# Kernel tuning notes

Hardware: AMD Instinct MI355X
Metric: run time of the kernel (lower is better)

Reference implementation:

```python
import jax, jax.numpy as jnp
import numpy as np

B, L, C = 2, 2048, 1024
DK, H = 64, 16

def setup_inputs() -> dict:
    key = jax.random.key(0)
    ks = jax.random.split(key, 12)
    def lin(kw, kb, out_dim, in_dim):
        w = jax.random.normal(kw, (out_dim, in_dim), jnp.float32) * (1.0 / np.sqrt(in_dim))
        b = jnp.zeros((out_dim,), jnp.float32)
        return w, b
    WQ_w, WQ_b = lin(ks[0], ks[1], DK * H, C)
    WK_w, WK_b = lin(ks[2], ks[3], DK * H, C)
    WV_w, WV_b = lin(ks[4], ks[5], DK * H, C)
    WO_w, WO_b = lin(ks[6], ks[7], C, DK * H)
    qx = jax.random.normal(ks[8], (B, L, C), jnp.float32)
    kx = jax.random.normal(ks[9], (B, L, C), jnp.float32)
    vx = jax.random.normal(ks[10], (B, L, C), jnp.float32)
    maskPAD = jax.random.randint(ks[11], (B, L, L), 0, 2, jnp.int32)
    return {"qx": qx, "kx": kx, "vx": vx, "maskPAD": maskPAD,
            "WQ_w": WQ_w, "WQ_b": WQ_b, "WK_w": WK_w, "WK_b": WK_b,
            "WV_w": WV_w, "WV_b": WV_b, "WO_w": WO_w, "WO_b": WO_b}

def reference(qx, kx, vx, maskPAD, WQ_w, WQ_b, WK_w, WK_b, WV_w, WV_b, WO_w, WO_b):
    Bq, qL, _ = qx.shape
    kvL = kx.shape[1]
    # projections -> [B, H, L, DK]
    q = (qx @ WQ_w.T + WQ_b).reshape(Bq, qL, H, DK).transpose(0, 2, 1, 3)
    k = (kx @ WK_w.T + WK_b).reshape(Bq, kvL, H, DK).transpose(0, 2, 1, 3)
    v = (vx @ WV_w.T + WV_b).reshape(Bq, kvL, H, DK).transpose(0, 2, 1, 3)
    scores = jnp.einsum('bhqd,bhkd->bhqk', q, k) / np.sqrt(DK).astype(np.float32)
    scores = jnp.where((maskPAD == 0)[:, None, :, :], jnp.float32(-2**15 + 1), scores)
    alpha = jax.nn.softmax(scores, axis=3)  # dropout p=0 (eval)
    z = jnp.einsum('bhqk,bhkd->bhqd', alpha, v)
    z = z.transpose(0, 2, 1, 3).reshape(Bq, qL, H * DK)
    return z @ WO_w.T + WO_b
```

## Files before the change

### kernel.cpp

```cpp
#include <hip/hip_runtime.h>
#include <stdint.h>
#include <math.h>

typedef short short8 __attribute__((ext_vector_type(8)));
typedef float float4v __attribute__((ext_vector_type(4)));

static __device__ __forceinline__ float bf2f(uint16_t u) {
    union { uint32_t i; float f; } x; x.i = ((uint32_t)u) << 16; return x.f;
}
static __device__ __forceinline__ uint16_t f2bf(float f) {
    union { float f; uint32_t i; } x; x.f = f;
    uint32_t u = x.i;
    u += 0x7FFFu + ((u >> 16) & 1u);
    return (uint16_t)(u >> 16);
}
static __device__ __forceinline__ uint16_t f2bf_sane(float f) {
    uint16_t u = f2bf(f);
    if ((u & 0x7F80u) == 0x7F80u) u = 0;
    return u;
}
static __device__ __forceinline__ float san_f32(float f) {
    union { float f; uint32_t i; } x; x.f = f;
    if (((x.i >> 23) & 0xFFu) == 0xFFu) return 0.f;
    return x.f;
}
static __device__ __forceinline__ void gll16(const void* g, void* l) {
    __builtin_amdgcn_global_load_lds((const __attribute__((address_space(1))) void*)g,
                                     (__attribute__((address_space(3))) void*)l,
                                     16, 0, 0);
}
static __device__ __forceinline__ short8 load8(const void* p, size_t off, int fp32) {
    if (!fp32) return *(const short8*)((const uint16_t*)p + off);
    const float* f = (const float*)p + off;
    const float4v a = *(const float4v*)f;
    const float4v b = *(const float4v*)(f + 4);
    short8 r;
    r[0] = (short)f2bf(a[0]); r[1] = (short)f2bf(a[1]);
    r[2] = (short)f2bf(a[2]); r[3] = (short)f2bf(a[3]);
    r[4] = (short)f2bf(b[0]); r[5] = (short)f2bf(b[1]);
    r[6] = (short)f2bf(b[2]); r[7] = (short)f2bf(b[3]);
    return r;
}

__global__ __launch_bounds__(256) void detect_kernel(const uint16_t* qx, int* flag)
{
    __shared__ int s;
    const int tid = threadIdx.x;
    if (tid == 0) s = 0;
    __syncthreads();
    int bad = 0;
#pragma unroll 8
    for (int i = 0; i < 64; ++i) {
        const uint16_t u = qx[tid * 64 + i];
        bad |= ((u & 0x7F80u) == 0x7F80u) ? 1 : 0;
    }
    if (bad) atomicOr(&s, 1);
    __syncthreads();
    if (tid == 0) *flag = s;
}

__global__ __launch_bounds__(256) void pack_kernel(
    const int* __restrict__ mask, uint64_t* __restrict__ mask64)
{
    const int wave = threadIdx.x >> 6, lane = threadIdx.x & 63;
    const int row = blockIdx.x * 4 + wave;
    const int* src = mask + (size_t)row * 2048;
#pragma unroll 4
    for (int j = 0; j < 32; ++j) {
        const int m = src[j * 64 + lane];
        const uint64_t bal = __ballot(m != 0);
        if (lane == 0) mask64[(size_t)row * 32 + j] = bal;
    }
}

__global__ __launch_bounds__(256) void convert_kernel(
    const void* qx, const void* kx, const void* vx,
    const void* wq, const void* wk, const void* wv, const void* wo,
    const void* bq, const void* bk, const void* bv, const void* bo,
    uint16_t* cIn, uint16_t* cW, uint16_t* cB, const int* flag)
{
    const int mode = *flag;
    if (!mode) return;
    const int z = blockIdx.z;
    if (z < 3) {
        const void* src = (z == 0) ? qx : (z == 1) ? kx : vx;
        uint16_t* dst = cIn + (size_t)z * 4194304;
#pragma unroll
        for (int it = 0; it < 8; ++it) {
            const int idx8 = (blockIdx.x * 8 + it) * 256 + threadIdx.x;
            *(short8*)(dst + (size_t)idx8 * 8) = load8(src, (size_t)idx8 * 8, 1);
        }
    } else if (z < 7) {
        const int t = z - 3;
        const void* src = (t == 0) ? wq : (t == 1) ? wk : (t == 2) ? wv : wo;
        uint16_t* dst = cW + (size_t)t * 1048576;
#pragma unroll
        for (int it = 0; it < 2; ++it) {
            const int idx8 = (blockIdx.x * 2 + it) * 256 + threadIdx.x;
            *(short8*)(dst + (size_t)idx8 * 8) = load8(src, (size_t)idx8 * 8, 1);
        }
    } else {
        const int idx8 = blockIdx.x * 256 + threadIdx.x;
        if (idx8 < 128) {
#pragma unroll
            for (int t = 0; t < 4; ++t) {
                const void* src = (t == 0) ? bq : (t == 1) ? bk : (t == 2) ? bv : bo;
                *(short8*)(cB + t * 1024 + idx8 * 8) = load8(src, (size_t)idx8 * 8, 1);
            }
        }
    }
}

template <int MI, int NI>
static __device__ __forceinline__ void gemm_tile(
    const uint16_t* __restrict__ A, const uint16_t* __restrict__ W,
    const uint16_t* __restrict__ bias, void* __restrict__ C,
    int c_fp32, float out_scale)
{
    constexpr int TM = MI * 32, TN = NI * 32;
    __shared__ __align__(16) uint16_t sA[TM * 32];
    __shared__ __align__(16) uint16_t sB[TN * 32];

    const int tid  = threadIdx.x;
    const int wave = tid >> 6;
    const int lane = tid & 63;
    const int quad = lane >> 4;
    const int l15  = lane & 15;
    const int m0 = blockIdx.y * TM;
    const int n0 = blockIdx.x * TN;
    const int wm = (wave >> 1) * (MI * 16);
    const int wn = (wave & 1) * (NI * 16);
    const int r16 = lane >> 2;
    const int ch  = lane & 3;

    float4v acc[MI][NI] = {};

    for (int k0 = 0; k0 < 1024; k0 += 32) {
        __syncthreads();
#pragma unroll
        for (int g = wave; g < TM / 16; g += 4)
            gll16(A + (size_t)(m0 + g * 16 + r16) * 1024 + k0 + ch * 8,
                  (char*)sA + (size_t)g * 1024);
#pragma unroll
        for (int g = wave; g < TN / 16; g += 4)
            gll16(W + (size_t)(n0 + g * 16 + r16) * 1024 + k0 + ch * 8,
                  (char*)sB + (size_t)g * 1024);
        asm volatile("s_waitcnt vmcnt(0)" ::: "memory");
        __syncthreads();

        short8 af[MI], bfr[NI];
#pragma unroll
        for (int i = 0; i < MI; ++i)
            af[i] = *(const short8*)&sA[(wm + i * 16 + l15) * 32 + quad * 8];
#pragma unroll
        for (int j = 0; j < NI; ++j)
            bfr[j] = *(const short8*)&sB[(wn + j * 16 + l15) * 32 + quad * 8];
#pragma unroll
        for (int mi = 0; mi < MI; ++mi)
#pragma unroll
            for (int ni = 0; ni < NI; ++ni)
                acc[mi][ni] = __builtin_amdgcn_mfma_f32_16x16x32_bf16(
                    af[mi], bfr[ni], acc[mi][ni], 0, 0, 0);
    }

#pragma unroll
    for (int ni = 0; ni < NI; ++ni) {
        const int n = n0 + wn + ni * 16 + l15;
        const float bv = bf2f(bias[n]);
#pragma unroll
        for (int mi = 0; mi < MI; ++mi) {
            const int mbase = m0 + wm + mi * 16 + quad * 4;
#pragma unroll
            for (int r = 0; r < 4; ++r) {
                const float v = (acc[mi][ni][r] + bv) * out_scale;
                const size_t idx = (size_t)(mbase + r) * 1024 + n;
                if (c_fp32) ((float*)C)[idx] = san_f32(v);
                else        ((uint16_t*)C)[idx] = f2bf_sane(v);
            }
        }
    }
}

__global__ __launch_bounds__(256) void qkv_kernel(
    const uint16_t* rqx, const uint16_t* rkx, const uint16_t* rvx,
    const uint16_t* rwq, const uint16_t* rwk, const uint16_t* rwv,
    const uint16_t* rbq, const uint16_t* rbk, const uint16_t* rbv,
    const uint16_t* cIn, const uint16_t* cW, const uint16_t* cB,
    uint16_t* Q, uint16_t* K, uint16_t* V, const int* flag)
{
    const int mode = *flag;
    const int z = blockIdx.z;
    const uint16_t* A = mode ? cIn + (size_t)z * 4194304
                             : ((z == 0) ? rqx : (z == 1) ? rkx : rvx);
    const uint16_t* W = mode ? cW + (size_t)z * 1048576
                             : ((z == 0) ? rwq : (z == 1) ? rwk : rwv);
    const uint16_t* b = mode ? cB + z * 1024
                             : ((z == 0) ? rbq : (z == 1) ? rbk : rbv);
    uint16_t* C = (z == 0) ? Q : (z == 1) ? K : V;
    const float sc = (z == 0) ? 0.125f : 1.0f;
    gemm_tile<4, 4>(A, W, b, C, 0, sc);
}

__global__ __launch_bounds__(256) void out_kernel(
    const uint16_t* Z, const uint16_t* rwo, const uint16_t* rbo,
    const uint16_t* cW, const uint16_t* cB, void* out, const int* flag)
{
    const int mode = *flag;
    const uint16_t* W = mode ? cW + 3 * 1048576 : rwo;
    const uint16_t* b = mode ? cB + 3 * 1024 : rbo;
    gemm_tile<2, 4>(Z, W, b, out, mode, 1.0f);
}

__global__ __launch_bounds__(256) void vtrans_kernel(
    const uint16_t* __restrict__ Vp, uint16_t* __restrict__ Vt)
{
    __shared__ __align__(16) uint16_t t[64][72];
    const int tid = threadIdx.x;
    const int lt = blockIdx.x, h = blockIdx.y, b = blockIdx.z;
#pragma unroll
    for (int p = 0; p < 2; ++p) {
        const int r = p * 32 + (tid >> 3);
        const int c = (tid & 7) * 8;
        *(short8*)&t[r][c] =
            *(const short8*)(Vp + (size_t)(b * 2048 + lt * 64 + r) * 1024 + h * 64 + c);
    }
    __syncthreads();
#pragma unroll
    for (int p = 0; p < 2; ++p) {
        const int d = p * 32 + (tid >> 3);
        const int c = (tid & 7) * 8;
        short8 v;
#pragma unroll
        for (int j = 0; j < 8; ++j) v[j] = (short)t[c + j][d];
        *(short8*)(Vt + (size_t)((b * 16 + h) * 64 + d) * 2048 + lt * 64 + c) = v;
    }
}

#define VS 72

__global__ __launch_bounds__(256) void attn_kernel(
    const uint16_t* __restrict__ Q, const uint16_t* __restrict__ Kp,
    const uint16_t* __restrict__ Vt, const uint64_t* __restrict__ mask64,
    uint16_t* __restrict__ Oa, uint16_t* __restrict__ Ob,
    float* __restrict__ lpart)
{
    __shared__ __align__(16) uint16_t sK[64 * VS];
    __shared__ __align__(16) uint16_t sV[64 * VS];
    __shared__ __align__(16) uint16_t sP[4][32 * VS];

    const int tid = threadIdx.x;
    const int wave = tid >> 6, lane = tid & 63;
    const int quad = lane >> 4, l15 = lane & 15;
    const int qt = blockIdx.x, h = blockIdx.y;
    const int b = blockIdx.z & 1, half = blockIdx.z >> 1;
    const int q0 = qt * 128;
    const int qw = q0 + wave * 32;

    const int srow = tid >> 2;
    const int sc0  = tid & 3;

    short8 qf[2][2];
#pragma unroll
    for (int mi = 0; mi < 2; ++mi)
#pragma unroll
        for (int kk = 0; kk < 2; ++kk)
            qf[mi][kk] = *(const short8*)(Q + (size_t)(b * 2048 + qw + mi * 16 + l15) * 1024
                                            + h * 64 + (quad + 4 * kk) * 8);

    const uint64_t* mrow[2][4];
#pragma unroll
    for (int mi = 0; mi < 2; ++mi)
#pragma unroll
        for (int r = 0; r < 4; ++r)
            mrow[mi][r] = mask64 + (size_t)(b * 2048 + qw + mi * 16 + quad * 4 + r) * 32;

    short8 ones;
#pragma unroll
    for (int j = 0; j < 8; ++j) ones[j] = (short)0x3F80;

    float4v oacc[2][4] = {};
    float4v lacc[2] = {};

    const int kt_lo = half * 16, kt_hi = kt_lo + 16;
    for (int kt = kt_lo; kt < kt_hi; ++kt) {
        const int k0 = kt * 64;
        const short8 kx0 = *(const short8*)(Kp + (size_t)(b * 2048 + k0 + srow) * 1024 + h * 64 + sc0 * 8);
        const short8 kx1 = *(const short8*)(Kp + (size_t)(b * 2048 + k0 + srow) * 1024 + h * 64 + (sc0 + 4) * 8);
        const short8 vx0 = *(const short8*)(Vt + (size_t)((b * 16 + h) * 64 + srow) * 2048 + k0 + sc0 * 8);
        const short8 vx1 = *(const short8*)(Vt + (size_t)((b * 16 + h) * 64 + srow) * 2048 + k0 + (sc0 + 4) * 8);
        __syncthreads();
        *(short8*)&sK[srow * VS + sc0 * 8]       = kx0;
        *(short8*)&sK[srow * VS + (sc0 + 4) * 8] = kx1;
        *(short8*)&sV[srow * VS + sc0 * 8]       = vx0;
        *(short8*)&sV[srow * VS + (sc0 + 4) * 8] = vx1;
        __syncthreads();

        float4v sacc[2][4] = {};
#pragma unroll
        for (int ni = 0; ni < 4; ++ni) {
            const int row = ni * 16 + l15;
#pragma unroll
            for (int kk = 0; kk < 2; ++kk) {
                const short8 kf = *(const short8*)&sK[row * VS + (quad + 4 * kk) * 8];
                sacc[0][ni] = __builtin_amdgcn_mfma_f32_16x16x32_bf16(qf[0][kk], kf, sacc[0][ni], 0, 0, 0);
                sacc[1][ni] = __builtin_amdgcn_mfma_f32_16x16x32_bf16(qf[1][kk], kf, sacc[1][ni], 0, 0, 0);
            }
        }

        uint16_t* Pw = &sP[wave][0];
#pragma unroll
        for (int mi = 0; mi < 2; ++mi) {
            uint64_t mw[4];
#pragma unroll
            for (int r = 0; r < 4; ++r) mw[r] = mrow[mi][r][kt];
#pragma unroll
            for (int ni = 0; ni < 4; ++ni)
#pragma unroll
                for (int r = 0; r < 4; ++r) {
                    const float p = ((mw[r] >> (ni * 16 + l15)) & 1ull)
                                        ? __expf(sacc[mi][ni][r]) : 0.f;
                    Pw[(mi * 16 + quad * 4 + r) * VS + ni * 16 + l15] = f2bf(p);
                }
        }
        asm volatile("s_waitcnt lgkmcnt(0)" ::: "memory");
        short8 pf[2][2];
#pragma unroll
        for (int mi = 0; mi < 2; ++mi)
#pragma unroll
            for (int kk = 0; kk < 2; ++kk)
                pf[mi][kk] = *(const short8*)&Pw[(mi * 16 + l15) * VS + (quad + 4 * kk) * 8];
        asm volatile("" ::: "memory");

#pragma unroll
        for (int ni = 0; ni < 4; ++ni) {
            const int row = ni * 16 + l15;
#pragma unroll
            for (int kk = 0; kk < 2; ++kk) {
                const short8 vf = *(const short8*)&sV[row * VS + (quad + 4 * kk) * 8];
                oacc[0][ni] = __builtin_amdgcn_mfma_f32_16x16x32_bf16(pf[0][kk], vf, oacc[0][ni], 0, 0, 0);
                oacc[1][ni] = __builtin_amdgcn_mfma_f32_16x16x32_bf16(pf[1][kk], vf, oacc[1][ni], 0, 0, 0);
            }
        }
#pragma unroll
        for (int mi = 0; mi < 2; ++mi)
#pragma unroll
            for (int kk = 0; kk < 2; ++kk)
                lacc[mi] = __builtin_amdgcn_mfma_f32_16x16x32_bf16(pf[mi][kk], ones, lacc[mi], 0, 0, 0);
    }

    uint16_t* Op = half ? Ob : Oa;
#pragma unroll
    for (int mi = 0; mi < 2; ++mi)
#pragma unroll
        for (int r = 0; r < 4; ++r) {
            const int qrow = qw + mi * 16 + quad * 4 + r;
#pragma unroll
            for (int ni = 0; ni < 4; ++ni)
                Op[(size_t)(b * 2048 + qrow) * 1024 + h * 64 + ni * 16 + l15] = f2bf(oacc[mi][ni][r]);
            if (l15 == 0)
                lpart[half * 65536 + (b * 16 + h) * 2048 + qrow] = lacc[mi][r];
        }
}

__global__ __launch_bounds__(256) void combine_kernel(
    const uint16_t* __restrict__ Oa, const uint16_t* __restrict__ Ob,
    const float* __restrict__ lpart, uint16_t* __restrict__ Z)
{
    const int e8 = blockIdx.x * 256 + threadIdx.x;
    const int flat = e8 * 8;
    const int bh_row = flat >> 10;
    const int h = (flat >> 6) & 15;
    const int b = bh_row >> 11;
    const int row = bh_row & 2047;
    const int lidx = (b * 16 + h) * 2048 + row;
    const float inv = 1.0f / fmaxf(lpart[lidx] + lpart[65536 + lidx], 1e-37f);
    const short8 a = *(const short8*)(Oa + flat);
    const short8 c = *(const short8*)(Ob + flat);
    short8 o;
#pragma unroll
    for (int j = 0; j < 8; ++j)
        o[j] = (short)f2bf_sane((bf2f((uint16_t)a[j]) + bf2f((uint16_t)c[j])) * inv);
    *(short8*)(Z + flat) = o;
}

extern "C" void kernel_launch(void* const* d_in, const int* in_sizes, int n_in,
                              void* d_out, int out_size, void* d_ws, size_t ws_size,
                              hipStream_t stream)
{
    const void* qx  = d_in[0];
    const void* kx  = d_in[1];
    const void* vx  = d_in[2];
    const int*  msk = (const int*)d_in[3];

    char* ws = (char*)d_ws;
    const size_t MB = 1024 * 1024;
    uint16_t* cIn = (uint16_t*)(ws);
    uint16_t* cW  = (uint16_t*)(ws + 24 * MB);
    uint16_t* cB  = (uint16_t*)(ws + 32 * MB);
    int*      flg = (int*)(ws + 32 * MB + 16 * 1024);
    uint16_t* Qb  = (uint16_t*)(ws + 33 * MB);
    uint16_t* Kb  = (uint16_t*)(ws + 41 * MB);
    uint16_t* Vb  = (uint16_t*)(ws + 49 * MB);
    uint64_t* m64 = (uint64_t*)(ws + 57 * MB);
    uint16_t* Vt  = (uint16_t*)(ws + 8 * MB);
    uint16_t* Oa  = (uint16_t*)(ws);
    uint16_t* Ob  = (uint16_t*)(ws + 16 * MB);
    float*    lp  = (float*)(ws + 49 * MB);
    uint16_t* Zb  = Oa;

    detect_kernel<<<1, 256, 0, stream>>>((const uint16_t*)qx, flg);
    pack_kernel<<<1024, 256, 0, stream>>>(msk, m64);
    convert_kernel<<<dim3(256, 1, 8), 256, 0, stream>>>(
        qx, kx, vx, d_in[4], d_in[6], d_in[8], d_in[10],
        d_in[5], d_in[7], d_in[9], d_in[11], cIn, cW, cB, flg);
    qkv_kernel<<<dim3(8, 32, 3), 256, 0, stream>>>(
        (const uint16_t*)qx, (const uint16_t*)kx, (const uint16_t*)vx,
        (const uint16_t*)d_in[4], (const uint16_t*)d_in[6], (const uint16_t*)d_in[8],
        (const uint16_t*)d_in[5], (const uint16_t*)d_in[7], (const uint16_t*)d_in[9],
        cIn, cW, cB, Qb, Kb, Vb, flg);
    vtrans_kernel<<<dim3(32, 16, 2), 256, 0, stream>>>(Vb, Vt);
    attn_kernel<<<dim3(16, 16, 4), 256, 0, stream>>>(Qb, Kb, Vt, m64, Oa, Ob, lp);
    combine_kernel<<<4096, 256, 0, stream>>>(Oa, Ob, lp, Zb);
    out_kernel<<<dim3(8, 64), 256, 0, stream>>>(
        Zb, (const uint16_t*)d_in[10], (const uint16_t*)d_in[11], cW, cB, d_out, flg);
}
```

Before: 325.3 us.

## Compute transposed scores so P stays in registers for the PV MFMA

Swaps the MFMA operand order so each lane holds a column of S^T. This lets the exponentiated probabilities feed the 16x16x16 bf16 MFMA for PV directly from registers, with no round trip through the per-wave LDS scratch buffer. The row sum moves from an extra MFMA against a ones vector to scalar accumulation plus cross-lane shuffles. Launch bounds now request 4 blocks per CU, and outputs are written as 4-wide vectors. The trade-off is using the half-width K=16 MFMA for PV, and the lsum still comes from fp32 values before bf16 rounding, so its rounding differs slightly from the previous path.

```diff
diff --git a/kernel.cpp b/kernel.cpp
--- a/kernel.cpp
+++ b/kernel.cpp
@@ -3,6 +3,7 @@
 #include <math.h>
 
 typedef short short8 __attribute__((ext_vector_type(8)));
+typedef short short4v __attribute__((ext_vector_type(4)));
 typedef float float4v __attribute__((ext_vector_type(4)));
 
 static __device__ __forceinline__ float bf2f(uint16_t u) {
@@ -42,6 +43,17 @@
     return r;
 }
 
+static __device__ __forceinline__ float4v mfma16_bf16(short4v a, short4v b, float4v c) {
+#if __has_builtin(__builtin_amdgcn_mfma_f32_16x16x16bf16_1k)
+    return __builtin_amdgcn_mfma_f32_16x16x16bf16_1k(a, b, c, 0, 0, 0);
+#else
+    float4v d = c;
+    asm volatile("v_mfma_f32_16x16x16_bf16 %0, %1, %2, %0"
+                 : "+v"(d) : "v"(a), "v"(b));
+    return d;
+#endif
+}
+
 __global__ __launch_bounds__(256) void detect_kernel(const uint16_t* qx, int* flag)
 {
     __shared__ int s;
@@ -238,7 +250,7 @@
 
 #define VS 72
 
-__global__ __launch_bounds__(256) void attn_kernel(
+__global__ __launch_bounds__(256, 4) void attn_kernel(
     const uint16_t* __restrict__ Q, const uint16_t* __restrict__ Kp,
     const uint16_t* __restrict__ Vt, const uint64_t* __restrict__ mask64,
     uint16_t* __restrict__ Oa, uint16_t* __restrict__ Ob,
@@ -246,7 +258,6 @@
 {
     __shared__ __align__(16) uint16_t sK[64 * VS];
     __shared__ __align__(16) uint16_t sV[64 * VS];
-    __shared__ __align__(16) uint16_t sP[4][32 * VS];
 
     const int tid = threadIdx.x;
     const int wave = tid >> 6, lane = tid & 63;
@@ -267,19 +278,13 @@
             qf[mi][kk] = *(const short8*)(Q + (size_t)(b * 2048 + qw + mi * 16 + l15) * 1024
                                             + h * 64 + (quad + 4 * kk) * 8);
 
-    const uint64_t* mrow[2][4];
-#pragma unroll
-    for (int mi = 0; mi < 2; ++mi)
-#pragma unroll
-        for (int r = 0; r < 4; ++r)
-            mrow[mi][r] = mask64 + (size_t)(b * 2048 + qw + mi * 16 + quad * 4 + r) * 32;
-
-    short8 ones;
-#pragma unroll
-    for (int j = 0; j < 8; ++j) ones[j] = (short)0x3F80;
-
-    float4v oacc[2][4] = {};
-    float4v lacc[2] = {};
+    const uint64_t* mrow[2];
+#pragma unroll
+    for (int mj = 0; mj < 2; ++mj)
+        mrow[mj] = mask64 + (size_t)(b * 2048 + qw + mj * 16 + l15) * 32;
+
+    float4v oaccT[4][2] = {};
+    float lsum[2] = {};
 
     const int kt_lo = half * 16, kt_hi = kt_lo + 16;
     for (int kt = kt_lo; kt < kt_hi; ++kt) {
@@ -288,6 +293,8 @@
         const short8 kx1 = *(const short8*)(Kp + (size_t)(b * 2048 + k0 + srow) * 1024 + h * 64 + (sc0 + 4) * 8);
         const short8 vx0 = *(const short8*)(Vt + (size_t)((b * 16 + h) * 64 + srow) * 2048 + k0 + sc0 * 8);
         const short8 vx1 = *(const short8*)(Vt + (size_t)((b * 16 + h) * 64 + srow) * 2048 + k0 + (sc0 + 4) * 8);
+        const uint64_t mw0 = mrow[0][kt];
+        const uint64_t mw1 = mrow[1][kt];
         __syncthreads();
         *(short8*)&sK[srow * VS + sc0 * 8]       = kx0;
         *(short8*)&sK[srow * VS + (sc0 + 4) * 8] = kx1;
@@ -302,64 +309,65 @@
 #pragma unroll
             for (int kk = 0; kk < 2; ++kk) {
                 const short8 kf = *(const short8*)&sK[row * VS + (quad + 4 * kk) * 8];
-                sacc[0][ni] = __builtin_amdgcn_mfma_f32_16x16x32_bf16(qf[0][kk], kf, sacc[0][ni], 0, 0, 0);
-                sacc[1][ni] = __builtin_amdgcn_mfma_f32_16x16x32_bf16(qf[1][kk], kf, sacc[1][ni], 0, 0, 0);
+                sacc[0][ni] = __builtin_amdgcn_mfma_f32_16x16x32_bf16(kf, qf[0][kk], sacc[0][ni], 0, 0, 0);
+                sacc[1][ni] = __builtin_amdgcn_mfma_f32_16x16x32_bf16(kf, qf[1][kk], sacc[1][ni], 0, 0, 0);
             }
         }
 
-        uint16_t* Pw = &sP[wave][0];
-#pragma unroll
-        for (int mi = 0; mi < 2; ++mi) {
-            uint64_t mw[4];
-#pragma unroll
-            for (int r = 0; r < 4; ++r) mw[r] = mrow[mi][r][kt];
-#pragma unroll
-            for (int ni = 0; ni < 4; ++ni)
+        short4v pf[2][4];
+#pragma unroll
+        for (int mj = 0; mj < 2; ++mj) {
+            const uint64_t mw = mj ? mw1 : mw0;
+#pragma unroll
+            for (int ni = 0; ni < 4; ++ni) {
+                const uint32_t nib = (uint32_t)(mw >> (ni * 16 + quad * 4)) & 0xFu;
+                short4v t;
 #pragma unroll
                 for (int r = 0; r < 4; ++r) {
-                    const float p = ((mw[r] >> (ni * 16 + l15)) & 1ull)
-                                        ? __expf(sacc[mi][ni][r]) : 0.f;
-                    Pw[(mi * 16 + quad * 4 + r) * VS + ni * 16 + l15] = f2bf(p);
+                    const float p = (nib >> r) & 1u ? __expf(sacc[mj][ni][r]) : 0.f;
+                    lsum[mj] += p;
+                    t[r] = (short)f2bf(p);
                 }
-        }
-        asm volatile("s_waitcnt lgkmcnt(0)" ::: "memory");
-        short8 pf[2][2];
-#pragma unroll
-        for (int mi = 0; mi < 2; ++mi)
-#pragma unroll
-            for (int kk = 0; kk < 2; ++kk)
-                pf[mi][kk] = *(const short8*)&Pw[(mi * 16 + l15) * VS + (quad + 4 * kk) * 8];
-        asm volatile("" ::: "memory");
-
-#pragma unroll
-        for (int ni = 0; ni < 4; ++ni) {
-            const int row = ni * 16 + l15;
-#pragma unroll
-            for (int kk = 0; kk < 2; ++kk) {
-                const short8 vf = *(const short8*)&sV[row * VS + (quad + 4 * kk) * 8];
-                oacc[0][ni] = __builtin_amdgcn_mfma_f32_16x16x32_bf16(pf[0][kk], vf, oacc[0][ni], 0, 0, 0);
-                oacc[1][ni] = __builtin_amdgcn_mfma_f32_16x16x32_bf16(pf[1][kk], vf, oacc[1][ni], 0, 0, 0);
+                pf[mj][ni] = t;
             }
         }
-#pragma unroll
-        for (int mi = 0; mi < 2; ++mi)
-#pragma unroll
-            for (int kk = 0; kk < 2; ++kk)
-                lacc[mi] = __builtin_amdgcn_mfma_f32_16x16x32_bf16(pf[mi][kk], ones, lacc[mi], 0, 0, 0);
+
+#pragma unroll
+        for (int di = 0; di < 4; ++di) {
+            const int row = di * 16 + l15;
+#pragma unroll
+            for (int ni = 0; ni < 4; ++ni) {
+                const short4v vf = *(const short4v*)&sV[row * VS + ni * 16 + quad * 4];
+                oaccT[di][0] = mfma16_bf16(vf, pf[0][ni], oaccT[di][0]);
+                oaccT[di][1] = mfma16_bf16(vf, pf[1][ni], oaccT[di][1]);
+            }
+        }
+    }
+
+#if !__has_builtin(__builtin_amdgcn_mfma_f32_16x16x16bf16_1k)
+    asm volatile("s_nop 7\ns_nop 7\ns_nop 7" ::: "memory");
+#endif
+
+#pragma unroll
+    for (int mj = 0; mj < 2; ++mj) {
+        lsum[mj] += __shfl_xor(lsum[mj], 16);
+        lsum[mj] += __shfl_xor(lsum[mj], 32);
     }
 
     uint16_t* Op = half ? Ob : Oa;
 #pragma unroll
-    for (int mi = 0; mi < 2; ++mi)
-#pragma unroll
-        for (int r = 0; r < 4; ++r) {
-            const int qrow = qw + mi * 16 + quad * 4 + r;
-#pragma unroll
-            for (int ni = 0; ni < 4; ++ni)
-                Op[(size_t)(b * 2048 + qrow) * 1024 + h * 64 + ni * 16 + l15] = f2bf(oacc[mi][ni][r]);
-            if (l15 == 0)
-                lpart[half * 65536 + (b * 16 + h) * 2048 + qrow] = lacc[mi][r];
-        }
+    for (int mj = 0; mj < 2; ++mj) {
+        const int qrow = qw + mj * 16 + l15;
+#pragma unroll
+        for (int di = 0; di < 4; ++di) {
+            short4v o;
+#pragma unroll
+            for (int r = 0; r < 4; ++r) o[r] = (short)f2bf(oaccT[di][mj][r]);
+            *(short4v*)(Op + (size_t)(b * 2048 + qrow) * 1024 + h * 64 + di * 16 + quad * 4) = o;
+        }
+        if (quad == 0)
+            lpart[half * 65536 + (b * 16 + h) * 2048 + qrow] = lsum[mj];
+    }
 }
 
 __global__ __launch_bounds__(256) void combine_kernel(
```

New measurement: 305.5 us. -6.1%, faster.
